# Kernel optimization log

Hardware: AMD Instinct MI355X
Metric: run time of the kernel (lower is better)

## Reference

```python
import jax, jax.numpy as jnp
import numpy as np

EPS = 1e-8


def setup_inputs() -> dict:
    key = jax.random.key(0)
    k1, k2 = jax.random.split(key)
    B, C, L = 16, 4, 4096
    K, S = 256, 128
    x = jax.random.normal(k1, (B, C, L), dtype=jnp.float32)
    shapelets = jax.random.normal(k2, (C, K, S), dtype=jnp.float32)
    return {"x": x, "shapelets": shapelets}


def reference(x, shapelets):
    # x: (B, C, L); shapelets: (C, K, S)
    B, C, L = x.shape
    _, K, S = shapelets.shape
    W = L - S + 1  # number of sliding windows

    # unfold: (B, C, W, S) sliding windows with stride 1
    idx = jnp.arange(W)[:, None] + jnp.arange(S)[None, :]  # (W, S)
    win = x[:, :, idx]  # (B, C, W, S)
    win = win / jnp.maximum(jnp.linalg.norm(win, axis=-1, keepdims=True), EPS)

    shp = shapelets / jnp.maximum(
        jnp.linalg.norm(shapelets, axis=-1, keepdims=True), EPS
    )  # (C, K, S)

    # pairwise dot products: (B, C, W, K)
    sim = jnp.einsum("bcws,cks->bcwk", win, shp)
    # sum over channels, keepdim, transpose(2,3), divide by n_dims
    sim = jnp.sum(sim, axis=1, keepdims=True) / C  # (B, 1, W, K)
    sim = jnp.transpose(sim, (0, 1, 3, 2))  # (B, 1, K, W)
    sim = jax.nn.relu(sim)
    # global max-pool over window positions -> (B, 1, K)
    return jnp.max(sim, axis=3)
```

## Files before the change

kernel.cpp:

```cpp
#include <hip/hip_runtime.h>
#include <hip/hip_bf16.h>

#define NB 16
#define NC 4
#define NL 4096
#define NK 256
#define NS 128
#define NW (NL - NS + 1)
#define WPB 128
#define NWT ((NW + WPB - 1) / WPB)
#define EPSF 1e-8f

typedef __attribute__((ext_vector_type(8))) short bf16x8;
typedef __attribute__((ext_vector_type(4))) float floatx4;

__device__ inline short f2bf(float f) {
    __hip_bfloat16 h = __float2bfloat16(f);
    short s;
    __builtin_memcpy(&s, &h, sizeof(short));
    return s;
}

__global__ __launch_bounds__(64)
void norm_shp_kernel(const float* __restrict__ shp, short* __restrict__ shpn) {
    int ck = blockIdx.x;
    int lane = threadIdx.x;
    const float* p = shp + (size_t)ck * NS;
    float v0 = p[lane];
    float v1 = p[lane + 64];
    float ss = v0 * v0 + v1 * v1;
    #pragma unroll
    for (int o = 32; o > 0; o >>= 1) ss += __shfl_xor(ss, o, 64);
    float rn = 1.f / fmaxf(sqrtf(ss), EPSF);
    shpn[(size_t)ck * NS + lane]      = f2bf(v0 * rn);
    shpn[(size_t)ck * NS + lane + 64] = f2bf(v1 * rn);
}

__global__ __launch_bounds__(256, 2)
void mcs_main_kernel(const float* __restrict__ x,
                     const short* __restrict__ shpn,
                     float* __restrict__ out) {
    __shared__ bf16x8 bs[NK * 16];
    __shared__ alignas(16) short xcp[NC][4][264];
    __shared__ alignas(16) float scratch[NC][264];
    __shared__ float invs[NC][WPB];

    const int wt = blockIdx.x, b = blockIdx.y;
    const int w0 = wt * WPB;
    const int tid = threadIdx.x;
    const int lane = tid & 63, wv = tid >> 6;

    float xv[NC];
    #pragma unroll
    for (int c = 0; c < NC; c++) {
        int g = w0 + tid;
        xv[c] = (g < NL) ? x[((size_t)b * NC + c) * NL + g] : 0.f;
    }
    bf16x8 breg[16];
    {
        const bf16x8* p = (const bf16x8*)shpn;
        #pragma unroll
        for (int i = 0; i < 16; i++) breg[i] = p[i * 256 + tid];
    }
    #pragma unroll
    for (int c = 0; c < NC; c++) {
        short hv = f2bf(xv[c]);
        #pragma unroll
        for (int r = 0; r < 4; r++) {
            int o2 = tid - r;
            if (o2 >= 0) xcp[c][r][o2] = hv;
        }
        scratch[c][tid] = xv[c] * xv[c];
    }
    __syncthreads();

    {
        float4 v = *(const float4*)&scratch[wv][lane * 4];
        v.y += v.x; v.z += v.y; v.w += v.z;
        float tot = v.w;
        #pragma unroll
        for (int o = 1; o < 64; o <<= 1) {
            float u = __shfl_up(tot, o, 64);
            if (lane >= o) tot += u;
        }
        float excl = tot - v.w;
        v.x += excl; v.y += excl; v.z += excl; v.w += excl;
        *(float4*)&scratch[wv][lane * 4] = v;
    }
    #pragma unroll
    for (int i = 0; i < 16; i++) {
        int g = i * 256 + tid;
        int k = g >> 4, cc = g & 15;
        bs[(k << 4) | (cc ^ (k & 15))] = breg[i];
    }
    __syncthreads();

    #pragma unroll
    for (int i = 0; i < 2; i++) {
        int idx = tid + 256 * i;
        int c = idx >> 7, o = idx & 127;
        float nn = scratch[c][o + 127] - (o ? scratch[c][o - 1] : 0.f);
        int w = w0 + o;
        invs[c][o] = (w < NW) ? 1.f / fmaxf(sqrtf(fmaxf(nn, 0.f)), EPSF) : 0.f;
    }
    __syncthreads();

    const int m = lane & 15, q = lane >> 4;
    const int kh = wv & 1, wh = wv >> 1;

    floatx4 acc[4][8];
    #pragma unroll
    for (int mt = 0; mt < 4; mt++)
        #pragma unroll
        for (int kt = 0; kt < 8; kt++) acc[mt][kt] = (floatx4){0.f, 0.f, 0.f, 0.f};

    const int r = m & 3;
    for (int c = 0; c < NC; c++) {
        if (c < NC - 1) {
            const bf16x8* p = (const bf16x8*)(shpn + (size_t)(c + 1) * NK * NS);
            #pragma unroll
            for (int i = 0; i < 16; i++) breg[i] = p[i * 256 + tid];
        }
        float im[4];
        #pragma unroll
        for (int mt = 0; mt < 4; mt++) im[mt] = invs[c][wh * 64 + mt * 16 + m];

        #pragma unroll
        for (int s0 = 0; s0 < NS; s0 += 32) {
            bf16x8 a[4];
            #pragma unroll
            for (int mt = 0; mt < 4; mt++) {
                int tt = wh * 64 + mt * 16 + m + s0 + q * 8;
                const uint2* pp = (const uint2*)&xcp[c][r][tt - r];
                uint2 u0 = pp[0], u1 = pp[1];
                float imv = im[mt];
                a[mt][0] = f2bf(__uint_as_float(u0.x << 16) * imv);
                a[mt][1] = f2bf(__uint_as_float(u0.x & 0xffff0000u) * imv);
                a[mt][2] = f2bf(__uint_as_float(u0.y << 16) * imv);
                a[mt][3] = f2bf(__uint_as_float(u0.y & 0xffff0000u) * imv);
                a[mt][4] = f2bf(__uint_as_float(u1.x << 16) * imv);
                a[mt][5] = f2bf(__uint_as_float(u1.x & 0xffff0000u) * imv);
                a[mt][6] = f2bf(__uint_as_float(u1.y << 16) * imv);
                a[mt][7] = f2bf(__uint_as_float(u1.y & 0xffff0000u) * imv);
            }
            int cc = (s0 >> 3) + q;
            #pragma unroll
            for (int kt = 0; kt < 8; kt++) {
                int k = kh * 128 + kt * 16 + m;
                bf16x8 bf = bs[(k << 4) | (cc ^ m)];
                #pragma unroll
                for (int mt = 0; mt < 4; mt++)
                    acc[mt][kt] = __builtin_amdgcn_mfma_f32_16x16x32_bf16(a[mt], bf, acc[mt][kt], 0, 0, 0);
            }
        }
        if (c < NC - 1) {
            __syncthreads();
            #pragma unroll
            for (int i = 0; i < 16; i++) {
                int g = i * 256 + tid;
                int k = g >> 4, cc = g & 15;
                bs[(k << 4) | (cc ^ (k & 15))] = breg[i];
            }
            __syncthreads();
        }
    }

    __syncthreads();
    #pragma unroll
    for (int kt = 0; kt < 8; kt++) {
        floatx4 v0 = acc[0][kt], v1 = acc[1][kt], v2 = acc[2][kt], v3 = acc[3][kt];
        float mx = fmaxf(fmaxf(fmaxf(v0.x, v0.y), fmaxf(v0.z, v0.w)),
                         fmaxf(fmaxf(v1.x, v1.y), fmaxf(v1.z, v1.w)));
        mx = fmaxf(mx, fmaxf(fmaxf(fmaxf(v2.x, v2.y), fmaxf(v2.z, v2.w)),
                             fmaxf(fmaxf(v3.x, v3.y), fmaxf(v3.z, v3.w))));
        mx = fmaxf(mx, __shfl_xor(mx, 16, 64));
        mx = fmaxf(mx, __shfl_xor(mx, 32, 64));
        if (lane < 16) scratch[wv][kt * 16 + lane] = mx;
    }
    __syncthreads();
    {
        int k = tid;
        int khh = k >> 7, lk = k & 127;
        float v = fmaxf(scratch[khh][lk], scratch[khh + 2][lk]);
        v = fmaxf(v, 0.f) * 0.25f;
        atomicMax((int*)out + (size_t)b * NK + k, __float_as_int(v));
    }
}

extern "C" void kernel_launch(void* const* d_in, const int* in_sizes, int n_in,
                              void* d_out, int out_size, void* d_ws, size_t ws_size,
                              hipStream_t stream) {
    (void)in_sizes; (void)n_in; (void)out_size; (void)ws_size;
    const float* x   = (const float*)d_in[0];
    const float* shp = (const float*)d_in[1];
    float* out = (float*)d_out;

    short* shpn = (short*)d_ws;

    norm_shp_kernel<<<NC * NK, 64, 0, stream>>>(shp, shpn);
    mcs_main_kernel<<<dim3(NWT, NB), 256, 0, stream>>>(x, shpn, out);
}
```

Baseline: 78.83 us.

## Fuse shapelet normalization into main kernel, split K across blocks, defer window scaling

Drops the separate shapelet-normalization kernel. Each block now loads raw fp32 shapelets, normalizes them and converts to bf16 inside the kernel, and double-buffers the shared B tile across channels so only one barrier is needed per channel. The K dimension is split over a second grid axis (128 shapelets per block), which doubles the block count and halves the accumulator registers. Window-norm scaling is moved out of the A-operand conversion into a per-channel post-MFMA multiply, so A fragments are plain bf16 loads. In exchange, shapelets are re-normalized redundantly in every block, and the raw bf16 inputs are no longer rounded after scaling, so numerics change slightly.

```diff
diff --git a/kernel.cpp b/kernel.cpp
--- a/kernel.cpp
+++ b/kernel.cpp
@@ -9,6 +9,7 @@
 #define NW (NL - NS + 1)
 #define WPB 128
 #define NWT ((NW + WPB - 1) / WPB)
+#define KPB 128
 #define EPSF 1e-8f
 
 typedef __attribute__((ext_vector_type(8))) short bf16x8;
@@ -21,46 +22,32 @@
     return s;
 }
 
-__global__ __launch_bounds__(64)
-void norm_shp_kernel(const float* __restrict__ shp, short* __restrict__ shpn) {
-    int ck = blockIdx.x;
-    int lane = threadIdx.x;
-    const float* p = shp + (size_t)ck * NS;
-    float v0 = p[lane];
-    float v1 = p[lane + 64];
-    float ss = v0 * v0 + v1 * v1;
-    #pragma unroll
-    for (int o = 32; o > 0; o >>= 1) ss += __shfl_xor(ss, o, 64);
-    float rn = 1.f / fmaxf(sqrtf(ss), EPSF);
-    shpn[(size_t)ck * NS + lane]      = f2bf(v0 * rn);
-    shpn[(size_t)ck * NS + lane + 64] = f2bf(v1 * rn);
-}
-
 __global__ __launch_bounds__(256, 2)
-void mcs_main_kernel(const float* __restrict__ x,
-                     const short* __restrict__ shpn,
-                     float* __restrict__ out) {
-    __shared__ bf16x8 bs[NK * 16];
+void mcs_kernel(const float* __restrict__ x,
+                const float* __restrict__ shp,
+                float* __restrict__ out) {
+    __shared__ bf16x8 bs[2][KPB * 16];
     __shared__ alignas(16) short xcp[NC][4][264];
     __shared__ alignas(16) float scratch[NC][264];
-    __shared__ float invs[NC][WPB];
+    __shared__ float invw[NC][WPB];
 
-    const int wt = blockIdx.x, b = blockIdx.y;
+    const int wt = blockIdx.x, kh2 = blockIdx.y, b = blockIdx.z;
     const int w0 = wt * WPB;
     const int tid = threadIdx.x;
     const int lane = tid & 63, wv = tid >> 6;
+
+    float4 f4[16];
+    {
+        const float4* bb = (const float4*)(shp + (size_t)(kh2 * KPB) * NS);
+        #pragma unroll
+        for (int i = 0; i < 16; i++) f4[i] = bb[i * 256 + tid];
+    }
 
     float xv[NC];
     #pragma unroll
     for (int c = 0; c < NC; c++) {
         int g = w0 + tid;
         xv[c] = (g < NL) ? x[((size_t)b * NC + c) * NL + g] : 0.f;
-    }
-    bf16x8 breg[16];
-    {
-        const bf16x8* p = (const bf16x8*)shpn;
-        #pragma unroll
-        for (int i = 0; i < 16; i++) breg[i] = p[i * 256 + tid];
     }
     #pragma unroll
     for (int c = 0; c < NC; c++) {
@@ -77,21 +64,15 @@
     {
         float4 v = *(const float4*)&scratch[wv][lane * 4];
         v.y += v.x; v.z += v.y; v.w += v.z;
-        float tot = v.w;
+        float tt = v.w;
         #pragma unroll
         for (int o = 1; o < 64; o <<= 1) {
-            float u = __shfl_up(tot, o, 64);
-            if (lane >= o) tot += u;
+            float u = __shfl_up(tt, o, 64);
+            if (lane >= o) tt += u;
         }
-        float excl = tot - v.w;
+        float excl = tt - v.w;
         v.x += excl; v.y += excl; v.z += excl; v.w += excl;
         *(float4*)&scratch[wv][lane * 4] = v;
-    }
-    #pragma unroll
-    for (int i = 0; i < 16; i++) {
-        int g = i * 256 + tid;
-        int k = g >> 4, cc = g & 15;
-        bs[(k << 4) | (cc ^ (k & 15))] = breg[i];
     }
     __syncthreads();
 
@@ -101,74 +82,92 @@
         int c = idx >> 7, o = idx & 127;
         float nn = scratch[c][o + 127] - (o ? scratch[c][o - 1] : 0.f);
         int w = w0 + o;
-        invs[c][o] = (w < NW) ? 1.f / fmaxf(sqrtf(fmaxf(nn, 0.f)), EPSF) : 0.f;
+        invw[c][o] = (w < NW) ? 1.f / fmaxf(sqrtf(fmaxf(nn, 0.f)), EPSF) : 0.f;
     }
+
+    auto stage_b = [&](int buf) {
+        #pragma unroll
+        for (int i = 0; i < 16; i++) {
+            float4 v = f4[i];
+            float ss = v.x * v.x + v.y * v.y + v.z * v.z + v.w * v.w;
+            #pragma unroll
+            for (int o = 1; o < 32; o <<= 1) ss += __shfl_xor(ss, o, 32);
+            float inv = 1.f / fmaxf(sqrtf(ss), EPSF);
+            int e = i * 1024 + tid * 4;
+            int k = e >> 7, u = (e >> 3) & 15, h = (e >> 2) & 1;
+            uint2 pw;
+            pw.x = (unsigned)(unsigned short)f2bf(v.x * inv)
+                 | ((unsigned)(unsigned short)f2bf(v.y * inv) << 16);
+            pw.y = (unsigned)(unsigned short)f2bf(v.z * inv)
+                 | ((unsigned)(unsigned short)f2bf(v.w * inv) << 16);
+            *(uint2*)((short*)&bs[buf][(k << 4) | (u ^ (k & 15))] + h * 4) = pw;
+        }
+    };
+    stage_b(0);
     __syncthreads();
 
-    const int m = lane & 15, q = lane >> 4;
+    const int m = lane & 15, q = lane >> 4, r = m & 3;
     const int kh = wv & 1, wh = wv >> 1;
 
-    floatx4 acc[4][8];
+    floatx4 tot[4][4];
     #pragma unroll
     for (int mt = 0; mt < 4; mt++)
         #pragma unroll
-        for (int kt = 0; kt < 8; kt++) acc[mt][kt] = (floatx4){0.f, 0.f, 0.f, 0.f};
+        for (int kt = 0; kt < 4; kt++) tot[mt][kt] = (floatx4){0.f, 0.f, 0.f, 0.f};
 
-    const int r = m & 3;
+    int cur = 0;
+    #pragma unroll
     for (int c = 0; c < NC; c++) {
         if (c < NC - 1) {
-            const bf16x8* p = (const bf16x8*)(shpn + (size_t)(c + 1) * NK * NS);
+            const float4* bb =
+                (const float4*)(shp + ((size_t)(c + 1) * NK + kh2 * KPB) * NS);
             #pragma unroll
-            for (int i = 0; i < 16; i++) breg[i] = p[i * 256 + tid];
+            for (int i = 0; i < 16; i++) f4[i] = bb[i * 256 + tid];
         }
-        float im[4];
-        #pragma unroll
-        for (int mt = 0; mt < 4; mt++) im[mt] = invs[c][wh * 64 + mt * 16 + m];
-
+        floatx4 part[4][4];
         #pragma unroll
         for (int s0 = 0; s0 < NS; s0 += 32) {
             bf16x8 a[4];
             #pragma unroll
             for (int mt = 0; mt < 4; mt++) {
-                int tt = wh * 64 + mt * 16 + m + s0 + q * 8;
-                const uint2* pp = (const uint2*)&xcp[c][r][tt - r];
-                uint2 u0 = pp[0], u1 = pp[1];
-                float imv = im[mt];
-                a[mt][0] = f2bf(__uint_as_float(u0.x << 16) * imv);
-                a[mt][1] = f2bf(__uint_as_float(u0.x & 0xffff0000u) * imv);
-                a[mt][2] = f2bf(__uint_as_float(u0.y << 16) * imv);
-                a[mt][3] = f2bf(__uint_as_float(u0.y & 0xffff0000u) * imv);
-                a[mt][4] = f2bf(__uint_as_float(u1.x << 16) * imv);
-                a[mt][5] = f2bf(__uint_as_float(u1.x & 0xffff0000u) * imv);
-                a[mt][6] = f2bf(__uint_as_float(u1.y << 16) * imv);
-                a[mt][7] = f2bf(__uint_as_float(u1.y & 0xffff0000u) * imv);
+                int ts = wh * 64 + mt * 16 + m + s0 + q * 8;
+                const uint2* pp = (const uint2*)&xcp[c][r][ts - r];
+                union { uint2 uu[2]; bf16x8 v; } cv;
+                cv.uu[0] = pp[0]; cv.uu[1] = pp[1];
+                a[mt] = cv.v;
             }
             int cc = (s0 >> 3) + q;
             #pragma unroll
-            for (int kt = 0; kt < 8; kt++) {
-                int k = kh * 128 + kt * 16 + m;
-                bf16x8 bf = bs[(k << 4) | (cc ^ m)];
+            for (int kt = 0; kt < 4; kt++) {
+                int k = kh * 64 + kt * 16 + m;
+                bf16x8 bf = bs[cur][(k << 4) | (cc ^ (k & 15))];
                 #pragma unroll
-                for (int mt = 0; mt < 4; mt++)
-                    acc[mt][kt] = __builtin_amdgcn_mfma_f32_16x16x32_bf16(a[mt], bf, acc[mt][kt], 0, 0, 0);
+                for (int mt = 0; mt < 4; mt++) {
+                    part[mt][kt] = (s0 == 0)
+                        ? __builtin_amdgcn_mfma_f32_16x16x32_bf16(
+                              a[mt], bf, (floatx4){0.f, 0.f, 0.f, 0.f}, 0, 0, 0)
+                        : __builtin_amdgcn_mfma_f32_16x16x32_bf16(
+                              a[mt], bf, part[mt][kt], 0, 0, 0);
+                }
             }
         }
+        #pragma unroll
+        for (int mt = 0; mt < 4; mt++) {
+            const float4 iv = *(const float4*)&invw[c][wh * 64 + mt * 16 + q * 4];
+            floatx4 ivv = (floatx4){iv.x, iv.y, iv.z, iv.w};
+            #pragma unroll
+            for (int kt = 0; kt < 4; kt++) tot[mt][kt] += ivv * part[mt][kt];
+        }
         if (c < NC - 1) {
+            stage_b(cur ^ 1);
             __syncthreads();
-            #pragma unroll
-            for (int i = 0; i < 16; i++) {
-                int g = i * 256 + tid;
-                int k = g >> 4, cc = g & 15;
-                bs[(k << 4) | (cc ^ (k & 15))] = breg[i];
-            }
-            __syncthreads();
+            cur ^= 1;
         }
     }
 
-    __syncthreads();
     #pragma unroll
-    for (int kt = 0; kt < 8; kt++) {
-        floatx4 v0 = acc[0][kt], v1 = acc[1][kt], v2 = acc[2][kt], v3 = acc[3][kt];
+    for (int kt = 0; kt < 4; kt++) {
+        floatx4 v0 = tot[0][kt], v1 = tot[1][kt], v2 = tot[2][kt], v3 = tot[3][kt];
         float mx = fmaxf(fmaxf(fmaxf(v0.x, v0.y), fmaxf(v0.z, v0.w)),
                          fmaxf(fmaxf(v1.x, v1.y), fmaxf(v1.z, v1.w)));
         mx = fmaxf(mx, fmaxf(fmaxf(fmaxf(v2.x, v2.y), fmaxf(v2.z, v2.w)),
@@ -178,25 +177,22 @@
         if (lane < 16) scratch[wv][kt * 16 + lane] = mx;
     }
     __syncthreads();
-    {
-        int k = tid;
-        int khh = k >> 7, lk = k & 127;
-        float v = fmaxf(scratch[khh][lk], scratch[khh + 2][lk]);
+    if (tid < 128) {
+        int khh = tid >> 6, j = tid & 63;
+        float v = fmaxf(scratch[khh][j], scratch[khh + 2][j]);
         v = fmaxf(v, 0.f) * 0.25f;
-        atomicMax((int*)out + (size_t)b * NK + k, __float_as_int(v));
+        int kg = kh2 * KPB + khh * 64 + j;
+        atomicMax((int*)out + (size_t)b * NK + kg, __float_as_int(v));
     }
 }
 
 extern "C" void kernel_launch(void* const* d_in, const int* in_sizes, int n_in,
                               void* d_out, int out_size, void* d_ws, size_t ws_size,
                               hipStream_t stream) {
-    (void)in_sizes; (void)n_in; (void)out_size; (void)ws_size;
+    (void)in_sizes; (void)n_in; (void)out_size; (void)d_ws; (void)ws_size;
     const float* x   = (const float*)d_in[0];
     const float* shp = (const float*)d_in[1];
     float* out = (float*)d_out;
 
-    short* shpn = (short*)d_ws;
-
-    norm_shp_kernel<<<NC * NK, 64, 0, stream>>>(shp, shpn);
-    mcs_main_kernel<<<dim3(NWT, NB), 256, 0, stream>>>(x, shpn, out);
+    mcs_kernel<<<dim3(NWT, 2, NB), 256, 0, stream>>>(x, shp, out);
 }
```

Result: slower. 146.6 us (+85.9%).
